# Performance work log

Measured on AMD Instinct MI355X. Metric: run time of the kernel, lower is better.

Reference implementation:

```python
import jax, jax.numpy as jnp
import numpy as np

G = 7  # number of winner/loser assets

def setup_inputs() -> dict:
    key = jax.random.key(0)
    x = jax.random.normal(key, (4096, 8192, 1), dtype=jnp.float32)
    return {"x": x}

def reference(x):
    # x: [B, I, 1] -> [B, I]
    x = jnp.squeeze(x, axis=-1)
    # descending sort (argsort of -x gives descending order); gather values consistently
    sorted_indices = jnp.argsort(-x, axis=-1)                      # [B, I]
    sorted_x = jnp.take_along_axis(x, sorted_indices, axis=-1)     # [B, I] descending
    winner = jax.nn.softmax(sorted_x[:, :G], axis=-1)              # [B, G]
    loser = -jax.nn.softmax(1.0 - sorted_x[:, -G:], axis=-1)       # [B, G]
    zeros_mid = jnp.zeros_like(sorted_x[:, G:-G])                  # [B, I-2G]
    b_c = jnp.concatenate([winner, zeros_mid, loser], axis=1)      # [B, I]
    return (b_c, sorted_indices)
```

## Files before the change

### kernel.cpp

```cpp
#include <hip/hip_runtime.h>
#include <stdint.h>

#define N 8192
#define G 7
#define T 512
#define NW 8
typedef uint32_t u32;
typedef uint16_t u16;

__device__ __forceinline__ u32 enc_desc(float x) {
    u32 u = __float_as_uint(x);
    return (u & 0x80000000u) ? u : (~u & 0x7FFFFFFFu);
}
__device__ __forceinline__ float dec_desc(u32 k) {
    u32 u = (k & 0x80000000u) ? k : (~k & 0x7FFFFFFFu);
    return __uint_as_float(u);
}

__global__ __launch_bounds__(T) void portfolio_radix_kernel(
    const float* __restrict__ x,
    float* __restrict__ bc,
    float* __restrict__ idx_out)
{
    __shared__ u32 val_s[N];
    __shared__ u16 idx_s[N];
    __shared__ u16 wcnt[NW * 256];
    __shared__ u16 dsum[256];
    __shared__ u32 wsum[4];

    const int t    = threadIdx.x;
    const int w    = t >> 6;
    const int lane = t & 63;
    const int row  = blockIdx.x;
    const float* xr  = x + (size_t)row * N;
    float* bcr = bc + (size_t)row * N;
    float* ixr = idx_out + (size_t)row * N;

    u32* wcnt32 = (u32*)wcnt;

    u32 hi[16];
    u32 ii[16];
    u32 rnk[16];
#pragma unroll
    for (int j = 0; j < 16; ++j) {
        int e = (w << 10) | (j << 6) | lane;
        hi[j] = enc_desc(xr[e]);
        ii[j] = (u32)e;
    }
    wcnt32[(w << 7) + lane] = 0;
    wcnt32[(w << 7) + 64 + lane] = 0;

    for (int p = 0; p < 4; ++p) {
        const int shift = 8 * p;

#pragma unroll
        for (int j = 0; j < 16; ++j) {
            u32 d   = (hi[j] >> shift) & 255u;
            u32 sh  = (d & 1u) << 4;
            u32 ret = atomicAdd(&wcnt32[(w << 7) + (d >> 1)], 1u << sh);
            rnk[j]  = (ret >> sh) & 0xFFFFu;
        }
        __syncthreads();

        if (t < 256) {
            u32 run = 0;
#pragma unroll
            for (int ww = 0; ww < NW; ++ww) {
                u32 c = (u32)wcnt[(ww << 8) | t];
                wcnt[(ww << 8) | t] = (u16)run;
                run += c;
            }
            u32 v = run;
#pragma unroll
            for (int off = 1; off < 64; off <<= 1) {
                u32 u = __shfl_up(v, off, 64);
                if (lane >= off) v += u;
            }
            if (lane == 63) wsum[w] = v;
            dsum[t] = (u16)(v - run);
        }
        __syncthreads();

        {
            u32 a0 = wsum[0], a1 = wsum[1], a2 = wsum[2];
#pragma unroll
            for (int i = 0; i < 4; ++i) {
                int d = lane + (i << 6);
                u32 addv = (i > 0 ? a0 : 0u) + (i > 1 ? a1 : 0u) + (i > 2 ? a2 : 0u);
                wcnt[(w << 8) + d] = (u16)((u32)wcnt[(w << 8) + d] + (u32)dsum[d] + addv);
            }
        }
#pragma unroll
        for (int j = 0; j < 16; ++j) {
            u32 d   = (hi[j] >> shift) & 255u;
            u32 pos = rnk[j] + (u32)wcnt[(w << 8) + d];
            if (p < 3 || pos < G || pos >= N - G) val_s[pos] = hi[j];
            idx_s[pos] = (u16)ii[j];
        }
        asm volatile("" ::: "memory");
        wcnt32[(w << 7) + lane] = 0;
        wcnt32[(w << 7) + 64 + lane] = 0;
        __syncthreads();

        if (p < 3) {
#pragma unroll
            for (int j = 0; j < 16; ++j) {
                int e = (w << 10) | (j << 6) | lane;
                hi[j] = val_s[e];
                ii[j] = (u32)idx_s[e];
            }
        }
    }

#pragma unroll
    for (int j = 0; j < 16; ++j) {
        int e = (w << 10) | (j << 6) | lane;
        ixr[e] = (float)idx_s[e];
        bcr[e] = 0.0f;
    }
    if (t < G) {
        float s[G], ex[G], sum = 0.f;
#pragma unroll
        for (int g = 0; g < G; ++g) s[g] = dec_desc(val_s[g]);
        float m0 = s[0];
#pragma unroll
        for (int g = 0; g < G; ++g) { ex[g] = expf(s[g] - m0); sum += ex[g]; }
        bcr[t] = ex[t] / sum;
    }
    if (t >= T - G) {
        float s[G], ex[G], sum = 0.f;
#pragma unroll
        for (int g = 0; g < G; ++g) s[g] = dec_desc(val_s[N - G + g]);
        float m0 = -s[G - 1];
#pragma unroll
        for (int g = 0; g < G; ++g) { ex[g] = expf(-s[g] - m0); sum += ex[g]; }
        bcr[(N - T) + t] = -ex[t - (T - G)] / sum;
    }
}

extern "C" void kernel_launch(void* const* d_in, const int* in_sizes, int n_in,
                              void* d_out, int out_size, void* d_ws, size_t ws_size,
                              hipStream_t stream) {
    const float* x = (const float*)d_in[0];
    float* out = (float*)d_out;
    const int B = in_sizes[0] / N;
    float* bc  = out;
    float* idx = out + (size_t)B * N;
    portfolio_radix_kernel<<<B, T, 0, stream>>>(x, bc, idx);
}
```

Before: 460.7 us.

## Swizzle radix histogram layout to cut LDS bank conflicts and move zero stores early

Changes the packed 16-bit per-warp histogram layout so digits d and d+128 share a 32-bit word, with an XOR swizzle on the word index to spread atomics across LDS banks. The scan phase is restructured: the dsum array is removed, and the first 256 threads add their digit base directly into all eight warp columns, at the cost of an extra __syncthreads. The zero stores for the middle of bc are moved into the initial load loop so they can overlap with the radix passes instead of running in the epilogue.

```diff
diff --git a/kernel.cpp b/kernel.cpp
--- a/kernel.cpp
+++ b/kernel.cpp
@@ -17,6 +17,9 @@
     return __uint_as_float(u);
 }
 
+__device__ __forceinline__ u32 dig_word(u32 d) { return (d & 127u) ^ ((d >> 7) * 0x2Bu); }
+__device__ __forceinline__ u32 dig_col16(u32 d) { return (dig_word(d) << 1) | (d >> 7); }
+
 __global__ __launch_bounds__(T) void portfolio_radix_kernel(
     const float* __restrict__ x,
     float* __restrict__ bc,
@@ -24,8 +27,7 @@
 {
     __shared__ u32 val_s[N];
     __shared__ u16 idx_s[N];
-    __shared__ u16 wcnt[NW * 256];
-    __shared__ u16 dsum[256];
+    __shared__ u32 wcnt32[NW * 128];
     __shared__ u32 wsum[4];
 
     const int t    = threadIdx.x;
@@ -36,7 +38,7 @@
     float* bcr = bc + (size_t)row * N;
     float* ixr = idx_out + (size_t)row * N;
 
-    u32* wcnt32 = (u32*)wcnt;
+    u16* wcnt16 = (u16*)wcnt32;
 
     u32 hi[16];
     u32 ii[16];
@@ -46,6 +48,7 @@
         int e = (w << 10) | (j << 6) | lane;
         hi[j] = enc_desc(xr[e]);
         ii[j] = (u32)e;
+        if (e >= G && e < N - G) bcr[e] = 0.0f;
     }
     wcnt32[(w << 7) + lane] = 0;
     wcnt32[(w << 7) + 64 + lane] = 0;
@@ -56,18 +59,20 @@
 #pragma unroll
         for (int j = 0; j < 16; ++j) {
             u32 d   = (hi[j] >> shift) & 255u;
-            u32 sh  = (d & 1u) << 4;
-            u32 ret = atomicAdd(&wcnt32[(w << 7) + (d >> 1)], 1u << sh);
+            u32 sh  = (d >> 7) << 4;
+            u32 ret = atomicAdd(&wcnt32[(w << 7) + dig_word(d)], 1u << sh);
             rnk[j]  = (ret >> sh) & 0xFFFFu;
         }
         __syncthreads();
 
+        u32 vtot = 0, runv = 0;
         if (t < 256) {
+            const int col = (int)dig_col16((u32)t);
             u32 run = 0;
 #pragma unroll
             for (int ww = 0; ww < NW; ++ww) {
-                u32 c = (u32)wcnt[(ww << 8) | t];
-                wcnt[(ww << 8) | t] = (u16)run;
+                u32 c = (u32)wcnt16[(ww << 8) + col];
+                wcnt16[(ww << 8) + col] = (u16)run;
                 run += c;
             }
             u32 v = run;
@@ -77,23 +82,26 @@
                 if (lane >= off) v += u;
             }
             if (lane == 63) wsum[w] = v;
-            dsum[t] = (u16)(v - run);
+            vtot = v; runv = run;
         }
         __syncthreads();
 
-        {
-            u32 a0 = wsum[0], a1 = wsum[1], a2 = wsum[2];
+        if (t < 256) {
+            u32 dbase = vtot - runv;
+            if (w > 0) dbase += wsum[0];
+            if (w > 1) dbase += wsum[1];
+            if (w > 2) dbase += wsum[2];
+            const int col = (int)dig_col16((u32)t);
 #pragma unroll
-            for (int i = 0; i < 4; ++i) {
-                int d = lane + (i << 6);
-                u32 addv = (i > 0 ? a0 : 0u) + (i > 1 ? a1 : 0u) + (i > 2 ? a2 : 0u);
-                wcnt[(w << 8) + d] = (u16)((u32)wcnt[(w << 8) + d] + (u32)dsum[d] + addv);
-            }
+            for (int ww = 0; ww < NW; ++ww)
+                wcnt16[(ww << 8) + col] = (u16)((u32)wcnt16[(ww << 8) + col] + dbase);
         }
+        __syncthreads();
+
 #pragma unroll
         for (int j = 0; j < 16; ++j) {
             u32 d   = (hi[j] >> shift) & 255u;
-            u32 pos = rnk[j] + (u32)wcnt[(w << 8) + d];
+            u32 pos = rnk[j] + (u32)wcnt16[(w << 8) + dig_col16(d)];
             if (p < 3 || pos < G || pos >= N - G) val_s[pos] = hi[j];
             idx_s[pos] = (u16)ii[j];
         }
@@ -116,7 +124,6 @@
     for (int j = 0; j < 16; ++j) {
         int e = (w << 10) | (j << 6) | lane;
         ixr[e] = (float)idx_s[e];
-        bcr[e] = 0.0f;
     }
     if (t < G) {
         float s[G], ex[G], sum = 0.f;
```

New measurement: 442.8 us. -3.9%, faster.
